# Optimization experiments

Measured on AMD Instinct MI355X. Metric: run time of the kernel, lower is better.

The kernel has to match this reference:

```python
import jax, jax.numpy as jnp
import numpy as np

SEQ, BZ, DIM = 2048, 16, 1024
NUM_LANG, DICT_LEN = 16, 32000


def setup_inputs() -> dict:
    key = jax.random.key(0)
    ks = jax.random.split(key, 6)
    x = jax.random.normal(ks[0], (SEQ, BZ, DIM), dtype=jnp.float32)
    # raw language ids live at the tail of the dictionary: dict_len-1-raw in [0, num_lang)
    raw = DICT_LEN - 1 - jax.random.randint(ks[1], (BZ,), 0, NUM_LANG)
    W_base = jax.random.normal(ks[2], (DIM, DIM), dtype=jnp.float32) * (DIM ** -0.5)
    b_base = jax.random.normal(ks[3], (DIM,), dtype=jnp.float32) * 0.02
    W = jax.random.uniform(ks[4], (NUM_LANG, DIM, DIM), dtype=jnp.float32) * (DIM ** -0.5)
    bias = jax.random.uniform(ks[5], (NUM_LANG, DIM), dtype=jnp.float32)
    return {"x": x, "lang_ids": raw, "W_base": W_base, "b_base": b_base,
            "W": W, "bias": bias, "dict_len": DICT_LEN, "num_lang": NUM_LANG}


def reference(x, lang_ids, W_base, b_base, W, bias, dict_len, num_lang):
    # Map raw ids to expert indices in [0, num_lang)
    ids = dict_len - 1 - lang_ids                      # [bz]
    # base_model (nn.Linear): h = x @ W_base.T + b_base
    h = jnp.einsum('sbd,ed->sbe', x, W_base) + b_base  # [seq, bz, dim]
    # The original pads each language group to max group size, runs a batched
    # einsum 'abcd,ade->abce' over languages, then scatters back with per-lang
    # bias. Mathematically each batch column j gets W[lang_j] applied:
    We = W[ids]                                        # [bz, dim, dim]
    out = jnp.einsum('sbd,bde->sbe', h, We) + bias[ids][None, :, :]
    return out
```

## Files before the change

kernel.cpp:

```cpp
#include <hip/hip_runtime.h>
#include <stdint.h>

typedef unsigned short u16;
typedef unsigned int u32;
typedef __bf16 bf16x8 __attribute__((ext_vector_type(8)));
typedef float f32x4 __attribute__((ext_vector_type(4)));

#define SEQ 2048
#define BZ 16
#define DIM 1024

__device__ __forceinline__ u16 f2bf(float f) {
    union { float f; u32 u; } a; a.f = f;
    u32 r = a.u + 0x7FFFu + ((a.u >> 16) & 1u);
    return (u16)(r >> 16);
}
__device__ __forceinline__ float bf2f(u16 u) {
    union { u32 u; float f; } a; a.u = ((u32)u) << 16;
    return a.f;
}
__device__ __forceinline__ void async16(const u16* g, u16* l) {
    __builtin_amdgcn_global_load_lds(
        (const __attribute__((address_space(1))) void*)g,
        (__attribute__((address_space(3))) void*)l, 16, 0, 0);
}

__global__ void convert_x(const float* __restrict__ x, u16* __restrict__ xb)
{
    int s = blockIdx.x;
    int t = threadIdx.x;
    const float4* src = (const float4*)(x + (size_t)s * BZ * DIM);
    #pragma unroll
    for (int j = 0; j < 16; j++) {
        int idx = j * 256 + t;
        float4 v = src[idx];
        int e = idx * 4;
        int b = e >> 10, d = e & 1023;
        u32 lo = f2bf(v.x) | ((u32)f2bf(v.y) << 16);
        u32 hi = f2bf(v.z) | ((u32)f2bf(v.w) << 16);
        *(uint2*)(xb + ((size_t)b * SEQ + s) * DIM + d) = make_uint2(lo, hi);
    }
}

__global__ void transpose_cvt(const float* __restrict__ W,
                              const float* __restrict__ W_base,
                              const int* __restrict__ lang_ids,
                              const int* __restrict__ dict_len,
                              u16* __restrict__ Wt,
                              u16* __restrict__ Wbt)
{
    int z = blockIdx.z;
    const float* S;
    u16* D;
    if (z < BZ) {
        int id = dict_len[0] - 1 - lang_ids[z];
        S = W + (size_t)id * DIM * DIM;
        D = Wbt + (size_t)z * DIM * DIM;
    } else {
        S = W_base;
        D = Wt;
    }
    __shared__ float tile[32][33];
    int tx = threadIdx.x, ty = threadIdx.y;
    int x0 = blockIdx.x * 32, y0 = blockIdx.y * 32;
    #pragma unroll
    for (int i = 0; i < 4; i++)
        tile[ty + 8 * i][tx] = S[(size_t)(y0 + ty + 8 * i) * DIM + x0 + tx];
    __syncthreads();
    #pragma unroll
    for (int i = 0; i < 4; i++)
        D[(size_t)(x0 + ty + 8 * i) * DIM + y0 + tx] = f2bf(tile[tx][ty + 8 * i]);
}

__global__ void bb_kernel(const u16* __restrict__ Wbt,
                          const float* __restrict__ b_base,
                          const float* __restrict__ bias,
                          const int* __restrict__ lang_ids,
                          const int* __restrict__ dict_len,
                          float* __restrict__ bb)
{
    int gw = blockIdx.x * 4 + (threadIdx.x >> 6);
    int b = gw >> 10;
    int f = gw & 1023;
    int lane = threadIdx.x & 63;
    const u16* row = Wbt + ((size_t)b * DIM + f) * DIM;
    float s = 0.f;
    #pragma unroll
    for (int i = 0; i < DIM / 64; i++)
        s += bf2f(row[lane + 64 * i]) * b_base[lane + 64 * i];
    #pragma unroll
    for (int off = 32; off; off >>= 1)
        s += __shfl_xor(s, off, 64);
    if (lane == 0) {
        int id = dict_len[0] - 1 - lang_ids[b];
        bb[b * DIM + f] = s + bias[(size_t)id * DIM + f];
    }
}

__global__ void gemm1_kernel(const u16* __restrict__ Wbt,
                             const u16* __restrict__ Wt,
                             u16* __restrict__ CT)
{
    int b = blockIdx.z;
    int f0 = blockIdx.y * 128;
    int d0 = blockIdx.x * 128;
    const u16* A = Wbt + (size_t)b * DIM * DIM;
    const u16* B = Wt;
    u16* C = CT + (size_t)b * DIM * DIM;

    __shared__ u16 As[128 * 32];
    __shared__ u16 Bs[128 * 32];

    int tid = threadIdx.x;
    int wave = tid >> 6, lane = tid & 63;
    int wm = (wave >> 1) * 64, wn = (wave & 1) * 64;
    int quad = lane >> 4, lr = lane & 15;

    int srow = wave * 32 + (lane >> 2);
    int scol = (lane & 3) * 8;
    const u16* ga0 = A + (size_t)(f0 + srow) * DIM + scol;
    const u16* ga1 = ga0 + (size_t)16 * DIM;
    const u16* gb0 = B + (size_t)(d0 + srow) * DIM + scol;
    const u16* gb1 = gb0 + (size_t)16 * DIM;
    u16* la0 = &As[(wave * 32) * 32];
    u16* la1 = &As[(wave * 32 + 16) * 32];
    u16* lb0 = &Bs[(wave * 32) * 32];
    u16* lb1 = &Bs[(wave * 32 + 16) * 32];

    f32x4 acc[4][4];
    #pragma unroll
    for (int i = 0; i < 4; i++)
        #pragma unroll
        for (int j = 0; j < 4; j++)
            #pragma unroll
            for (int e = 0; e < 4; e++) acc[i][j][e] = 0.f;

    for (int k0 = 0; k0 < DIM; k0 += 32) {
        async16(ga0, la0); async16(ga1, la1);
        async16(gb0, lb0); async16(gb1, lb1);
        ga0 += 32; ga1 += 32; gb0 += 32; gb1 += 32;
        __syncthreads();
        bf16x8 af[4], bfv[4];
        #pragma unroll
        for (int mt = 0; mt < 4; mt++)
            af[mt] = *(const bf16x8*)&As[(wm + mt * 16 + lr) * 32 + quad * 8];
        #pragma unroll
        for (int nt = 0; nt < 4; nt++)
            bfv[nt] = *(const bf16x8*)&Bs[(wn + nt * 16 + lr) * 32 + quad * 8];
        #pragma unroll
        for (int mt = 0; mt < 4; mt++)
            #pragma unroll
            for (int nt = 0; nt < 4; nt++)
                acc[mt][nt] = __builtin_amdgcn_mfma_f32_16x16x32_bf16(
                    af[mt], bfv[nt], acc[mt][nt], 0, 0, 0);
        __syncthreads();
    }
    #pragma unroll
    for (int mt = 0; mt < 4; mt++) {
        int fr = f0 + wm + mt * 16 + quad * 4;
        #pragma unroll
        for (int nt = 0; nt < 4; nt++) {
            int dc = d0 + wn + nt * 16 + lr;
            #pragma unroll
            for (int rr = 0; rr < 4; rr++)
                C[(size_t)(fr + rr) * DIM + dc] = f2bf(acc[mt][nt][rr]);
        }
    }
}

__global__ void gemm2_kernel(const u16* __restrict__ xb,
                             const u16* __restrict__ CT,
                             const float* __restrict__ bb,
                             float* __restrict__ out)
{
    int b = blockIdx.z;
    int s0 = blockIdx.y * 128;
    int f0 = blockIdx.x * 128;
    const u16* A = xb + (size_t)b * SEQ * DIM;
    const u16* Bm = CT + (size_t)b * DIM * DIM;

    __shared__ u16 As[128 * 32];
    __shared__ u16 Bs[128 * 32];

    int tid = threadIdx.x;
    int wave = tid >> 6, lane = tid & 63;
    int wm = (wave >> 1) * 64, wn = (wave & 1) * 64;
    int quad = lane >> 4, lr = lane & 15;

    int srow = wave * 32 + (lane >> 2);
    int scol = (lane & 3) * 8;
    const u16* ga0 = A + (size_t)(s0 + srow) * DIM + scol;
    const u16* ga1 = ga0 + (size_t)16 * DIM;
    const u16* gb0 = Bm + (size_t)(f0 + srow) * DIM + scol;
    const u16* gb1 = gb0 + (size_t)16 * DIM;
    u16* la0 = &As[(wave * 32) * 32];
    u16* la1 = &As[(wave * 32 + 16) * 32];
    u16* lb0 = &Bs[(wave * 32) * 32];
    u16* lb1 = &Bs[(wave * 32 + 16) * 32];

    f32x4 acc[4][4];
    #pragma unroll
    for (int i = 0; i < 4; i++)
        #pragma unroll
        for (int j = 0; j < 4; j++)
            #pragma unroll
            for (int e = 0; e < 4; e++) acc[i][j][e] = 0.f;

    for (int k0 = 0; k0 < DIM; k0 += 32) {
        async16(ga0, la0); async16(ga1, la1);
        async16(gb0, lb0); async16(gb1, lb1);
        ga0 += 32; ga1 += 32; gb0 += 32; gb1 += 32;
        __syncthreads();
        bf16x8 af[4], bfv[4];
        #pragma unroll
        for (int mt = 0; mt < 4; mt++)
            af[mt] = *(const bf16x8*)&As[(wm + mt * 16 + lr) * 32 + quad * 8];
        #pragma unroll
        for (int nt = 0; nt < 4; nt++)
            bfv[nt] = *(const bf16x8*)&Bs[(wn + nt * 16 + lr) * 32 + quad * 8];
        #pragma unroll
        for (int mt = 0; mt < 4; mt++)
            #pragma unroll
            for (int nt = 0; nt < 4; nt++)
                acc[mt][nt] = __builtin_amdgcn_mfma_f32_16x16x32_bf16(
                    af[mt], bfv[nt], acc[mt][nt], 0, 0, 0);
        __syncthreads();
    }
    #pragma unroll
    for (int nt = 0; nt < 4; nt++) {
        int fcol = f0 + wn + nt * 16 + lr;
        float bv = bb[b * DIM + fcol];
        #pragma unroll
        for (int mt = 0; mt < 4; mt++) {
            int sr = s0 + wm + mt * 16 + quad * 4;
            #pragma unroll
            for (int rr = 0; rr < 4; rr++)
                out[((size_t)(sr + rr) * BZ + b) * DIM + fcol] = acc[mt][nt][rr] + bv;
        }
    }
}

extern "C" void kernel_launch(void* const* d_in, const int* in_sizes, int n_in,
                              void* d_out, int out_size, void* d_ws, size_t ws_size,
                              hipStream_t stream)
{
    const float* x        = (const float*)d_in[0];
    const int*   lang_ids = (const int*)d_in[1];
    const float* W_base   = (const float*)d_in[2];
    const float* b_base   = (const float*)d_in[3];
    const float* W        = (const float*)d_in[4];
    const float* bias     = (const float*)d_in[5];
    const int*   dict_len = (const int*)d_in[6];
    float* out = (float*)d_out;

    char* ws = (char*)d_ws;
    u16*  Wt  = (u16*)ws;
    u16*  Wbt = (u16*)(ws + (size_t)(2u << 20));
    u16*  CT  = (u16*)(ws + (size_t)(34u << 20));
    float* bb = (float*)(ws + (size_t)(66u << 20));
    u16*  xb  = (u16*)(ws + (size_t)(67u << 20));

    convert_x<<<dim3(SEQ, 1, 1), 256, 0, stream>>>(x, xb);
    transpose_cvt<<<dim3(32, 32, 17), dim3(32, 8, 1), 0, stream>>>(
        W, W_base, lang_ids, dict_len, Wt, Wbt);
    bb_kernel<<<dim3(4096, 1, 1), 256, 0, stream>>>(
        Wbt, b_base, bias, lang_ids, dict_len, bb);
    gemm1_kernel<<<dim3(8, 8, 16), 256, 0, stream>>>(Wbt, Wt, CT);
    gemm2_kernel<<<dim3(8, 16, 16), 256, 0, stream>>>(xb, CT, bb, out);
}
```

Baseline: 453.6 us.

## Fuse prep kernels into one launch, swizzle LDS, remap blocks per XCD

Merges x conversion, weight transpose/convert and bias-fold computation into a single prep kernel. The bias fold now reads fp32 W directly instead of the transposed bf16 copy, which removes the dependency on the transpose. The two GEMMs get an XOR swizzle on LDS columns to cut bank conflicts, plus a 1D grid that maps each batch to one XCD for L2 locality. The new bias path does strided column reads over the full fp32 W per expert, which adds memory traffic, and one thread computes 1024 sequential FMAs.

```diff
diff --git a/kernel.cpp b/kernel.cpp
--- a/kernel.cpp
+++ b/kernel.cpp
@@ -15,85 +15,75 @@
     u32 r = a.u + 0x7FFFu + ((a.u >> 16) & 1u);
     return (u16)(r >> 16);
 }
-__device__ __forceinline__ float bf2f(u16 u) {
-    union { u32 u; float f; } a; a.u = ((u32)u) << 16;
-    return a.f;
-}
 __device__ __forceinline__ void async16(const u16* g, u16* l) {
     __builtin_amdgcn_global_load_lds(
         (const __attribute__((address_space(1))) void*)g,
         (__attribute__((address_space(3))) void*)l, 16, 0, 0);
 }
 
-__global__ void convert_x(const float* __restrict__ x, u16* __restrict__ xb)
-{
-    int s = blockIdx.x;
-    int t = threadIdx.x;
-    const float4* src = (const float4*)(x + (size_t)s * BZ * DIM);
-    #pragma unroll
-    for (int j = 0; j < 16; j++) {
-        int idx = j * 256 + t;
-        float4 v = src[idx];
-        int e = idx * 4;
-        int b = e >> 10, d = e & 1023;
-        u32 lo = f2bf(v.x) | ((u32)f2bf(v.y) << 16);
-        u32 hi = f2bf(v.z) | ((u32)f2bf(v.w) << 16);
-        *(uint2*)(xb + ((size_t)b * SEQ + s) * DIM + d) = make_uint2(lo, hi);
-    }
-}
-
-__global__ void transpose_cvt(const float* __restrict__ W,
-                              const float* __restrict__ W_base,
-                              const int* __restrict__ lang_ids,
-                              const int* __restrict__ dict_len,
-                              u16* __restrict__ Wt,
-                              u16* __restrict__ Wbt)
-{
-    int z = blockIdx.z;
-    const float* S;
-    u16* D;
-    if (z < BZ) {
-        int id = dict_len[0] - 1 - lang_ids[z];
-        S = W + (size_t)id * DIM * DIM;
-        D = Wbt + (size_t)z * DIM * DIM;
+__global__ void prep_kernel(const float* __restrict__ x,
+                            const float* __restrict__ W,
+                            const float* __restrict__ W_base,
+                            const float* __restrict__ b_base,
+                            const float* __restrict__ bias,
+                            const int* __restrict__ lang_ids,
+                            const int* __restrict__ dict_len,
+                            u16* __restrict__ xb,
+                            u16* __restrict__ Wt,
+                            u16* __restrict__ Wbt,
+                            float* __restrict__ bb)
+{
+    __shared__ float tile[32][33];
+    int u = blockIdx.x;
+    int tid = threadIdx.x;
+
+    if (u < 2048) {
+        int s = u;
+        const float4* src = (const float4*)(x + (size_t)s * BZ * DIM);
+        #pragma unroll
+        for (int j = 0; j < 16; j++) {
+            int idx = j * 256 + tid;
+            float4 v = src[idx];
+            int e = idx * 4;
+            int b = e >> 10, d = e & 1023;
+            u32 lo = f2bf(v.x) | ((u32)f2bf(v.y) << 16);
+            u32 hi = f2bf(v.z) | ((u32)f2bf(v.w) << 16);
+            *(uint2*)(xb + ((size_t)b * SEQ + s) * DIM + d) = make_uint2(lo, hi);
+        }
+    } else if (u < 19456) {
+        int t = u - 2048;
+        int z = t >> 10;
+        int w = t & 1023;
+        int x0 = (w & 31) * 32, y0 = (w >> 5) * 32;
+        const float* S;
+        u16* D;
+        if (z < BZ) {
+            int id = dict_len[0] - 1 - lang_ids[z];
+            S = W + (size_t)id * DIM * DIM;
+            D = Wbt + (size_t)z * DIM * DIM;
+        } else {
+            S = W_base;
+            D = Wt;
+        }
+        int tx = tid & 31, ty = tid >> 5;
+        #pragma unroll
+        for (int i = 0; i < 4; i++)
+            tile[ty + 8 * i][tx] = S[(size_t)(y0 + ty + 8 * i) * DIM + x0 + tx];
+        __syncthreads();
+        #pragma unroll
+        for (int i = 0; i < 4; i++)
+            D[(size_t)(x0 + ty + 8 * i) * DIM + y0 + tx] = f2bf(tile[tx][ty + 8 * i]);
     } else {
-        S = W_base;
-        D = Wt;
-    }
-    __shared__ float tile[32][33];
-    int tx = threadIdx.x, ty = threadIdx.y;
-    int x0 = blockIdx.x * 32, y0 = blockIdx.y * 32;
-    #pragma unroll
-    for (int i = 0; i < 4; i++)
-        tile[ty + 8 * i][tx] = S[(size_t)(y0 + ty + 8 * i) * DIM + x0 + tx];
-    __syncthreads();
-    #pragma unroll
-    for (int i = 0; i < 4; i++)
-        D[(size_t)(x0 + ty + 8 * i) * DIM + y0 + tx] = f2bf(tile[tx][ty + 8 * i]);
-}
-
-__global__ void bb_kernel(const u16* __restrict__ Wbt,
-                          const float* __restrict__ b_base,
-                          const float* __restrict__ bias,
-                          const int* __restrict__ lang_ids,
-                          const int* __restrict__ dict_len,
-                          float* __restrict__ bb)
-{
-    int gw = blockIdx.x * 4 + (threadIdx.x >> 6);
-    int b = gw >> 10;
-    int f = gw & 1023;
-    int lane = threadIdx.x & 63;
-    const u16* row = Wbt + ((size_t)b * DIM + f) * DIM;
-    float s = 0.f;
-    #pragma unroll
-    for (int i = 0; i < DIM / 64; i++)
-        s += bf2f(row[lane + 64 * i]) * b_base[lane + 64 * i];
-    #pragma unroll
-    for (int off = 32; off; off >>= 1)
-        s += __shfl_xor(s, off, 64);
-    if (lane == 0) {
+        int v = u - 19456;
+        int b = v >> 2;
+        int f = (v & 3) * 256 + tid;
         int id = dict_len[0] - 1 - lang_ids[b];
-        bb[b * DIM + f] = s + bias[(size_t)id * DIM + f];
+        const float* Wp = W + (size_t)id * DIM * DIM + f;
+        float acc = 0.f;
+        #pragma unroll 4
+        for (int e = 0; e < DIM; e++)
+            acc += b_base[e] * Wp[(size_t)e * DIM];
+        bb[b * DIM + f] = acc + bias[(size_t)id * DIM + f];
     }
 }
 
@@ -101,9 +91,14 @@
                              const u16* __restrict__ Wt,
                              u16* __restrict__ CT)
 {
-    int b = blockIdx.z;
-    int f0 = blockIdx.y * 128;
-    int d0 = blockIdx.x * 128;
+    int id0 = blockIdx.x;
+    int xcd = id0 & 7;
+    int i = id0 >> 3;
+    int b = xcd + 8 * (i >> 6);
+    int j = i & 63;
+    int d0 = (j & 7) * 128;
+    int f0 = (j >> 3) * 128;
+
     const u16* A = Wbt + (size_t)b * DIM * DIM;
     const u16* B = Wt;
     u16* C = CT + (size_t)b * DIM * DIM;
@@ -115,9 +110,10 @@
     int wave = tid >> 6, lane = tid & 63;
     int wm = (wave >> 1) * 64, wn = (wave & 1) * 64;
     int quad = lane >> 4, lr = lane & 15;
+    int sq = (quad ^ (lr & 3)) * 8;
 
     int srow = wave * 32 + (lane >> 2);
-    int scol = (lane & 3) * 8;
+    int scol = 8 * ((lane & 3) ^ ((lane >> 2) & 3));
     const u16* ga0 = A + (size_t)(f0 + srow) * DIM + scol;
     const u16* ga1 = ga0 + (size_t)16 * DIM;
     const u16* gb0 = B + (size_t)(d0 + srow) * DIM + scol;
@@ -129,11 +125,11 @@
 
     f32x4 acc[4][4];
     #pragma unroll
-    for (int i = 0; i < 4; i++)
-        #pragma unroll
-        for (int j = 0; j < 4; j++)
-            #pragma unroll
-            for (int e = 0; e < 4; e++) acc[i][j][e] = 0.f;
+    for (int mi = 0; mi < 4; mi++)
+        #pragma unroll
+        for (int nj = 0; nj < 4; nj++)
+            #pragma unroll
+            for (int e = 0; e < 4; e++) acc[mi][nj][e] = 0.f;
 
     for (int k0 = 0; k0 < DIM; k0 += 32) {
         async16(ga0, la0); async16(ga1, la1);
@@ -143,10 +139,10 @@
         bf16x8 af[4], bfv[4];
         #pragma unroll
         for (int mt = 0; mt < 4; mt++)
-            af[mt] = *(const bf16x8*)&As[(wm + mt * 16 + lr) * 32 + quad * 8];
+            af[mt] = *(const bf16x8*)&As[(wm + mt * 16 + lr) * 32 + sq];
         #pragma unroll
         for (int nt = 0; nt < 4; nt++)
-            bfv[nt] = *(const bf16x8*)&Bs[(wn + nt * 16 + lr) * 32 + quad * 8];
+            bfv[nt] = *(const bf16x8*)&Bs[(wn + nt * 16 + lr) * 32 + sq];
         #pragma unroll
         for (int mt = 0; mt < 4; mt++)
             #pragma unroll
@@ -173,9 +169,14 @@
                              const float* __restrict__ bb,
                              float* __restrict__ out)
 {
-    int b = blockIdx.z;
-    int s0 = blockIdx.y * 128;
-    int f0 = blockIdx.x * 128;
+    int id0 = blockIdx.x;
+    int xcd = id0 & 7;
+    int i = id0 >> 3;
+    int b = xcd + 8 * (i >> 7);
+    int j = i & 127;
+    int f0 = (j & 7) * 128;
+    int s0 = (j >> 3) * 128;
+
     const u16* A = xb + (size_t)b * SEQ * DIM;
     const u16* Bm = CT + (size_t)b * DIM * DIM;
 
@@ -186,9 +187,10 @@
     int wave = tid >> 6, lane = tid & 63;
     int wm = (wave >> 1) * 64, wn = (wave & 1) * 64;
     int quad = lane >> 4, lr = lane & 15;
+    int sq = (quad ^ (lr & 3)) * 8;
 
     int srow = wave * 32 + (lane >> 2);
-    int scol = (lane & 3) * 8;
+    int scol = 8 * ((lane & 3) ^ ((lane >> 2) & 3));
     const u16* ga0 = A + (size_t)(s0 + srow) * DIM + scol;
     const u16* ga1 = ga0 + (size_t)16 * DIM;
     const u16* gb0 = Bm + (size_t)(f0 + srow) * DIM + scol;
@@ -200,11 +202,11 @@
 
     f32x4 acc[4][4];
     #pragma unroll
-    for (int i = 0; i < 4; i++)
-        #pragma unroll
-        for (int j = 0; j < 4; j++)
-            #pragma unroll
-            for (int e = 0; e < 4; e++) acc[i][j][e] = 0.f;
+    for (int mi = 0; mi < 4; mi++)
+        #pragma unroll
+        for (int nj = 0; nj < 4; nj++)
+            #pragma unroll
+            for (int e = 0; e < 4; e++) acc[mi][nj][e] = 0.f;
 
     for (int k0 = 0; k0 < DIM; k0 += 32) {
         async16(ga0, la0); async16(ga1, la1);
@@ -214,10 +216,10 @@
         bf16x8 af[4], bfv[4];
         #pragma unroll
         for (int mt = 0; mt < 4; mt++)
-            af[mt] = *(const bf16x8*)&As[(wm + mt * 16 + lr) * 32 + quad * 8];
+            af[mt] = *(const bf16x8*)&As[(wm + mt * 16 + lr) * 32 + sq];
         #pragma unroll
         for (int nt = 0; nt < 4; nt++)
-            bfv[nt] = *(const bf16x8*)&Bs[(wn + nt * 16 + lr) * 32 + quad * 8];
+            bfv[nt] = *(const bf16x8*)&Bs[(wn + nt * 16 + lr) * 32 + sq];
         #pragma unroll
         for (int mt = 0; mt < 4; mt++)
             #pragma unroll
@@ -260,11 +262,8 @@
     float* bb = (float*)(ws + (size_t)(66u << 20));
     u16*  xb  = (u16*)(ws + (size_t)(67u << 20));
 
-    convert_x<<<dim3(SEQ, 1, 1), 256, 0, stream>>>(x, xb);
-    transpose_cvt<<<dim3(32, 32, 17), dim3(32, 8, 1), 0, stream>>>(
-        W, W_base, lang_ids, dict_len, Wt, Wbt);
-    bb_kernel<<<dim3(4096, 1, 1), 256, 0, stream>>>(
-        Wbt, b_base, bias, lang_ids, dict_len, bb);
-    gemm1_kernel<<<dim3(8, 8, 16), 256, 0, stream>>>(Wbt, Wt, CT);
-    gemm2_kernel<<<dim3(8, 16, 16), 256, 0, stream>>>(xb, CT, bb, out);
-}
+    prep_kernel<<<dim3(19520, 1, 1), 256, 0, stream>>>(
+        x, W, W_base, b_base, bias, lang_ids, dict_len, xb, Wt, Wbt, bb);
+    gemm1_kernel<<<dim3(1024, 1, 1), 256, 0, stream>>>(Wbt, Wt, CT);
+    gemm2_kernel<<<dim3(2048, 1, 1), 256, 0, stream>>>(xb, CT, bb, out);
+}
```

Result: slower. 494.7 us (+9.1%).
